# Kernel tuning notes

Measured on AMD Instinct MI355X. Metric: run time of the kernel, lower is better.

The kernel has to match this reference:

```python
import jax, jax.numpy as jnp
import numpy as np

N_NODES = 100_000
N_EDGES = 1_600_000
D = 128  # in = hidden = out channels
LAYERS = 3


def setup_inputs() -> dict:
    key = jax.random.key(0)
    ks = jax.random.split(key, 16)
    inp = {
        "x": jax.random.normal(ks[0], (N_NODES, D), dtype=jnp.float32),
        "edge_weight": jax.random.uniform(ks[1], (N_EDGES,), dtype=jnp.float32),
    }
    scale = 1.0 / np.sqrt(D)
    for l in range(LAYERS):
        inp[f"W_rel_{l}"] = jax.random.normal(ks[2 + 3 * l], (D, D), dtype=jnp.float32) * scale
        inp[f"W_root_{l}"] = jax.random.normal(ks[3 + 3 * l], (D, D), dtype=jnp.float32) * scale
        inp[f"b_{l}"] = jax.random.normal(ks[4 + 3 * l], (D,), dtype=jnp.float32) * scale
    inp["edge_src"] = jax.random.randint(ks[11], (N_EDGES,), 0, N_NODES, dtype=jnp.int32)
    inp["edge_dst"] = jax.random.randint(ks[12], (N_EDGES,), 0, N_NODES, dtype=jnp.int32)
    return inp


def _graph_conv(h, edge_src, edge_dst, edge_weight, W_rel, W_root, b):
    # PyG GraphConv: out_i = W_root @ h_i + W_rel @ (sum_{j->i} w_ji * h_j) + b
    msg = h[edge_src] * edge_weight[:, None]                      # [E, D] gather
    agg = jax.ops.segment_sum(msg, edge_dst, num_segments=h.shape[0])  # [N, D] scatter-add
    return agg @ W_rel.T + h @ W_root.T + b


def reference(x, edge_weight, W_rel_0, W_root_0, b_0, W_rel_1, W_root_1, b_1,
              W_rel_2, W_root_2, b_2, edge_src, edge_dst):
    h = _graph_conv(x, edge_src, edge_dst, edge_weight, W_rel_0, W_root_0, b_0)
    h = jax.nn.relu(h)
    h = _graph_conv(h, edge_src, edge_dst, edge_weight, W_rel_1, W_root_1, b_1)
    h = jax.nn.relu(h)
    h = _graph_conv(h, edge_src, edge_dst, edge_weight, W_rel_2, W_root_2, b_2)
    return h
```

## Files before the change

kernel.cpp:

```cpp
#include <hip/hip_runtime.h>

#define N_NODES 100000
#define N_EDGES 1600000
#define D 128
#define GEMM_GRID 6250
#define TILE_ROWS 16
#define BK_NODES 256
#define N_BUCKETS 391
#define BKT_CAP 5120
#define SC_BLOCKS 128
#define EPB 12500

typedef _Float16 f16;
typedef _Float16 f16x8 __attribute__((ext_vector_type(8)));
typedef _Float16 f16x2 __attribute__((ext_vector_type(2)));
typedef float f32x2 __attribute__((ext_vector_type(2)));
typedef float f32x4 __attribute__((ext_vector_type(4)));

__device__ __forceinline__ unsigned bf16bits(float x) {
    unsigned u = __float_as_uint(x);
    return ((u + 0x8000u) >> 16) & 0x7fffu;
}


__global__ __launch_bounds__(256) void bucket_scatter(const int* __restrict__ src,
                                                      const int* __restrict__ dst,
                                                      const float* __restrict__ w,
                                                      int* __restrict__ bcur,
                                                      int2* __restrict__ bkt) {
    __shared__ int hist[N_BUCKETS];
    __shared__ int base[N_BUCKETS];
    int tid = threadIdx.x;
    int v0  = blockIdx.x * (EPB / 4);
    const int4*   dst4 = (const int4*)dst;
    const int4*   src4 = (const int4*)src;
    const float4* w4   = (const float4*)w;

    for (int b = tid; b < N_BUCKETS; b += 256) hist[b] = 0;
    __syncthreads();

    for (int v = tid; v < EPB / 4; v += 256) {
        int4 d = dst4[v0 + v];
        atomicAdd(&hist[d.x >> 8], 1);
        atomicAdd(&hist[d.y >> 8], 1);
        atomicAdd(&hist[d.z >> 8], 1);
        atomicAdd(&hist[d.w >> 8], 1);
    }
    __syncthreads();

    for (int b = tid; b < N_BUCKETS; b += 256) {
        int c = hist[b];
        base[b] = b * BKT_CAP + ((c > 0) ? atomicAdd(&bcur[b], c) : 0);
        hist[b] = 0;
    }
    __syncthreads();

    for (int v = tid; v < EPB / 4; v += 256) {
        int4   d = dst4[v0 + v];
        int4   s = src4[v0 + v];
        float4 f = w4[v0 + v];
        {
            int p = base[d.x >> 8] + atomicAdd(&hist[d.x >> 8], 1);
            bkt[p] = make_int2(s.x, (int)(((unsigned)d.x << 15) | bf16bits(f.x)));
        }
        {
            int p = base[d.y >> 8] + atomicAdd(&hist[d.y >> 8], 1);
            bkt[p] = make_int2(s.y, (int)(((unsigned)d.y << 15) | bf16bits(f.y)));
        }
        {
            int p = base[d.z >> 8] + atomicAdd(&hist[d.z >> 8], 1);
            bkt[p] = make_int2(s.z, (int)(((unsigned)d.z << 15) | bf16bits(f.z)));
        }
        {
            int p = base[d.w >> 8] + atomicAdd(&hist[d.w >> 8], 1);
            bkt[p] = make_int2(s.w, (int)(((unsigned)d.w << 15) | bf16bits(f.w)));
        }
    }
}

__global__ __launch_bounds__(512) void bucket_scan(const int* __restrict__ bcnt,
                                                   int* __restrict__ bbase) {
    __shared__ int sc[512];
    int tid = threadIdx.x;
    int v = (tid < N_BUCKETS) ? bcnt[tid] : 0;
    sc[tid] = v;
    __syncthreads();
    for (int off = 1; off < 512; off <<= 1) {
        int t = (tid >= off) ? sc[tid - off] : 0;
        __syncthreads();
        sc[tid] += t;
        __syncthreads();
    }
    if (tid < N_BUCKETS) bbase[tid] = sc[tid] - v;
}

__global__ __launch_bounds__(256) void bucket_finalize(const int* __restrict__ bcnt,
                                                       const int* __restrict__ bbase,
                                                       const int2* __restrict__ bkt,
                                                       unsigned* __restrict__ csr,
                                                       int* __restrict__ row_ptr) {
    __shared__ int ncnt[BK_NODES];
    __shared__ int noff[BK_NODES];
    __shared__ int sc[BK_NODES];
    int tid   = threadIdx.x;
    int b     = blockIdx.x;
    int node0 = b * BK_NODES;
    int cnt   = bcnt[b];
    int base  = bbase[b];
    int e0    = b * BKT_CAP;

    ncnt[tid] = 0;
    __syncthreads();
    for (int i = tid; i < cnt; i += 256) {
        int local = (int)((unsigned)bkt[e0 + i].y >> 15) - node0;
        atomicAdd(&ncnt[local], 1);
    }
    __syncthreads();
    int s = ncnt[tid];
    sc[tid] = s;
    __syncthreads();
    for (int off = 1; off < 256; off <<= 1) {
        int t = (tid >= off) ? sc[tid - off] : 0;
        __syncthreads();
        sc[tid] += t;
        __syncthreads();
    }
    noff[tid] = sc[tid] - s;
    ncnt[tid] = 0;
    {
        int nN = N_NODES - node0; if (nN > BK_NODES) nN = BK_NODES;
        if (tid < nN) row_ptr[node0 + tid] = base + noff[tid];
        if (b == N_BUCKETS - 1 && tid == 0) row_ptr[N_NODES] = N_EDGES;
    }
    __syncthreads();
    for (int i = tid; i < cnt; i += 256) {
        int2 t = bkt[e0 + i];
        unsigned meta = (unsigned)t.y;
        int local = (int)(meta >> 15) - node0;
        int p = base + noff[local] + atomicAdd(&ncnt[local], 1);
        csr[p] = ((unsigned)t.x << 15) | (meta & 0x7fffu);
    }
}


__global__ __launch_bounds__(256) void cvt_x(const float* __restrict__ in,
                                             f16* __restrict__ out16,
                                             unsigned char* __restrict__ out8) {
    int i = blockIdx.x * 256 + threadIdx.x;
    const float4* in4 = (const float4*)in;
    float4 a = in4[i * 2], b = in4[i * 2 + 1];
    f16x8 v;
    v[0] = (f16)a.x; v[1] = (f16)a.y; v[2] = (f16)a.z; v[3] = (f16)a.w;
    v[4] = (f16)b.x; v[5] = (f16)b.y; v[6] = (f16)b.z; v[7] = (f16)b.w;
    ((f16x8*)out16)[i] = v;
    uint2 p8;
    int r = __builtin_amdgcn_cvt_pk_fp8_f32(a.x, a.y, 0, false);
    r     = __builtin_amdgcn_cvt_pk_fp8_f32(a.z, a.w, r, true);
    p8.x = (unsigned)r;
    r     = __builtin_amdgcn_cvt_pk_fp8_f32(b.x, b.y, 0, false);
    r     = __builtin_amdgcn_cvt_pk_fp8_f32(b.z, b.w, r, true);
    p8.y = (unsigned)r;
    ((uint2*)out8)[i] = p8;
}


__global__ __launch_bounds__(256) void pack_weights(const float* __restrict__ Wrel,
                                                    const float* __restrict__ Wroot,
                                                    f16* __restrict__ Bp) {
    int idx = blockIdx.x * 256 + threadIdx.x;
    int e = idx & 7, lane = (idx >> 3) & 63, ct = (idx >> 9) & 7, ks = idx >> 12;
    int j = ct * 16 + (lane & 15);
    int k = ks * 32 + (lane >> 4) * 8 + e;
    float w = (k < D) ? Wrel[j * D + k] : Wroot[j * D + (k - D)];
    Bp[idx] = (f16)w;
}


#define FMA8(CWV)                                                              \
    {                                                                          \
        float w = __uint_as_float(((CWV) & 0x7fffu) << 16);                    \
        f32x2 c0 = __builtin_amdgcn_cvt_pk_f32_fp8((int)rv[j].x, false);       \
        f32x2 c1 = __builtin_amdgcn_cvt_pk_f32_fp8((int)rv[j].x, true);        \
        f32x2 c2 = __builtin_amdgcn_cvt_pk_f32_fp8((int)rv[j].y, false);       \
        f32x2 c3 = __builtin_amdgcn_cvt_pk_f32_fp8((int)rv[j].y, true);        \
        a0 = fmaf(w, c0.x, a0); a1 = fmaf(w, c0.y, a1);                        \
        a2 = fmaf(w, c1.x, a2); a3 = fmaf(w, c1.y, a3);                        \
        a4 = fmaf(w, c2.x, a4); a5 = fmaf(w, c2.y, a5);                        \
        a6 = fmaf(w, c3.x, a6); a7 = fmaf(w, c3.y, a7);                        \
    }

template <int FINAL>
__global__ __launch_bounds__(256) void fused_layer(const f16* __restrict__ h,
                                                   const unsigned char* __restrict__ h8,
                                                   const int* __restrict__ row_ptr,
                                                   const unsigned* __restrict__ csr,
                                                   const f16x8* __restrict__ Bp,
                                                   const float* __restrict__ bias,
                                                   void* __restrict__ outp,
                                                   unsigned char* __restrict__ outp8) {
    __shared__ f16 sA[TILE_ROWS * 256];
    int tid  = threadIdx.x;
    int lane = tid & 63;
    int wid  = tid >> 6;
    int node0 = blockIdx.x * TILE_ROWS;
    const uint4* h16 = (const uint4*)h;

    int quad = lane >> 4;
    int ql   = lane & 15;
    unsigned qoff = (unsigned)ql * 8u;

    {
        int row  = wid * 4 + quad;
        int node = node0 + row;
        int beg = row_ptr[node], end = row_ptr[node + 1];

        float a0 = 0.f, a1 = 0.f, a2 = 0.f, a3 = 0.f;
        float a4 = 0.f, a5 = 0.f, a6 = 0.f, a7 = 0.f;

        int e = beg;
        unsigned cw[8];
        if (e + 8 <= end) {
#pragma unroll
            for (int j = 0; j < 8; ++j) cw[j] = csr[e + j];
        }
        while (e + 8 <= end) {
            uint2 rv[8];
            __builtin_amdgcn_sched_barrier(0);
#pragma unroll
            for (int j = 0; j < 8; ++j) {
                unsigned off = ((cw[j] >> 8) & 0xFFFFFF80u) | qoff;
                rv[j] = *(const uint2*)(h8 + off);
            }
            unsigned cwn[8];
            bool more = (e + 16 <= end);
            if (more) {
#pragma unroll
                for (int j = 0; j < 8; ++j) cwn[j] = csr[e + 8 + j];
            }
            __builtin_amdgcn_sched_barrier(0);
#pragma unroll
            for (int j = 0; j < 8; ++j) FMA8(cw[j]);
            if (more) {
#pragma unroll
                for (int j = 0; j < 8; ++j) cw[j] = cwn[j];
            }
            e += 8;
        }
        if (e < end) {
            int rem = end - e;
            int em1 = end - 1;
            unsigned sm[8];
            uint2 rv[8];
#pragma unroll
            for (int j = 0; j < 8; ++j) {
                int idx = e + j; idx = idx < em1 ? idx : em1;
                unsigned c = csr[idx];
                sm[j] = (j < rem) ? c : 0u;
            }
            __builtin_amdgcn_sched_barrier(0);
#pragma unroll
            for (int j = 0; j < 8; ++j) {
                unsigned off = ((sm[j] >> 8) & 0xFFFFFF80u) | qoff;
                rv[j] = *(const uint2*)(h8 + off);
            }
            __builtin_amdgcn_sched_barrier(0);
#pragma unroll
            for (int j = 0; j < 8; ++j) FMA8(sm[j]);
        }
        f16x8 ov;
        ov[0] = (f16)a0; ov[1] = (f16)a1; ov[2] = (f16)a2; ov[3] = (f16)a3;
        ov[4] = (f16)a4; ov[5] = (f16)a5; ov[6] = (f16)a6; ov[7] = (f16)a7;
        int o = (row * 256 + ql * 8) ^ ((row & 7) << 3);
        *(f16x8*)&sA[o] = ov;
    }

    {
        int r = tid >> 4, c8 = (tid & 15) + 16;
        int o = (r * 256 + c8 * 8) ^ ((r & 7) << 3);
        *(uint4*)&sA[o] = h16[(size_t)(node0 + r) * 16 + (c8 - 16)];
    }
    __syncthreads();

    float bv[2];
#pragma unroll
    for (int c = 0; c < 2; ++c) bv[c] = bias[wid * 32 + c * 16 + (lane & 15)];

    f32x4 acc[2] = {f32x4{0,0,0,0}, f32x4{0,0,0,0}};
    int arow = lane & 15;
    int kg   = (lane >> 4) * 8;

    f16x8 b0 = Bp[(0 * 8 + wid * 2 + 0) * 64 + lane];
    f16x8 b1 = Bp[(0 * 8 + wid * 2 + 1) * 64 + lane];
#pragma unroll 1
    for (int ks = 0; ks < 8; ++ks) {
        f16x8 n0, n1;
        if (ks < 7) {
            n0 = Bp[((ks + 1) * 8 + wid * 2 + 0) * 64 + lane];
            n1 = Bp[((ks + 1) * 8 + wid * 2 + 1) * 64 + lane];
        }
        int o = (arow * 256 + ks * 32 + kg) ^ ((arow & 7) << 3);
        f16x8 afrag = *(const f16x8*)&sA[o];
        acc[0] = __builtin_amdgcn_mfma_f32_16x16x32_f16(afrag, b0, acc[0], 0, 0, 0);
        acc[1] = __builtin_amdgcn_mfma_f32_16x16x32_f16(afrag, b1, acc[1], 0, 0, 0);
        b0 = n0; b1 = n1;
    }

#pragma unroll
    for (int c = 0; c < 2; ++c) {
        int col = wid * 32 + c * 16 + (lane & 15);
#pragma unroll
        for (int r = 0; r < 4; ++r) {
            int row = node0 + (lane >> 4) * 4 + r;
            float o = acc[c][r] + bv[c];
            if (FINAL) {
                ((float*)outp)[(size_t)row * D + col] = o;
            } else {
                o = fmaxf(o, 0.f);
                ((f16*)outp)[(size_t)row * D + col] = (f16)o;
                int pk = __builtin_amdgcn_cvt_pk_fp8_f32(o, o, 0, false);
                outp8[(size_t)row * D + col] = (unsigned char)(pk & 0xff);
            }
        }
    }
}


extern "C" void kernel_launch(void* const* d_in, const int* in_sizes, int n_in,
                              void* d_out, int out_size, void* d_ws, size_t ws_size,
                              hipStream_t stream) {
    const float* x  = (const float*)d_in[0];
    const float* ew = (const float*)d_in[1];
    const float* W_rel[3]  = {(const float*)d_in[2], (const float*)d_in[5], (const float*)d_in[8]};
    const float* W_root[3] = {(const float*)d_in[3], (const float*)d_in[6], (const float*)d_in[9]};
    const float* bias[3]   = {(const float*)d_in[4], (const float*)d_in[7], (const float*)d_in[10]};
    const int* esrc = (const int*)d_in[11];
    const int* edst = (const int*)d_in[12];

    char* ws = (char*)d_ws;
    f16*           bufA16  = (f16*)           (ws);
    unsigned char* bufA8   = (unsigned char*) (ws + 25600000);
    f16*           bufB16  = (f16*)           (ws + 38400000);
    unsigned char* bufB8   = (unsigned char*) (ws + 64000000);
    unsigned*      csr     = (unsigned*)      (ws + 76800000);
    int2*          bkt     = (int2*)          (ws + 83200000);
    int*           row_ptr = (int*)           (ws + 99215360);
    int*           bcur    = (int*)           (ws + 99615376);
    int*           bbase   = (int*)           (ws + 99616940);
    f16*           Bp      = (f16*)           (ws + 99618504);

    hipMemsetAsync(bcur, 0, N_BUCKETS * sizeof(int), stream);
    bucket_scatter<<<SC_BLOCKS, 256, 0, stream>>>(esrc, edst, ew, bcur, bkt);
    bucket_scan<<<1, 512, 0, stream>>>(bcur, bbase);
    bucket_finalize<<<N_BUCKETS, 256, 0, stream>>>(bcur, bbase, bkt, csr, row_ptr);

    cvt_x<<<6250, 256, 0, stream>>>(x, bufA16, bufA8);
    for (int l = 0; l < 3; ++l)
        pack_weights<<<128, 256, 0, stream>>>(W_rel[l], W_root[l], Bp + l * 32768);

    fused_layer<0><<<GEMM_GRID, 256, 0, stream>>>(bufA16, bufA8, row_ptr, csr,
                                                  (const f16x8*)(Bp + 0 * 32768),
                                                  bias[0], bufB16, bufB8);
    fused_layer<0><<<GEMM_GRID, 256, 0, stream>>>(bufB16, bufB8, row_ptr, csr,
                                                  (const f16x8*)(Bp + 1 * 32768),
                                                  bias[1], bufA16, bufA8);
    fused_layer<1><<<GEMM_GRID, 256, 0, stream>>>(bufA16, bufA8, row_ptr, csr,
                                                  (const f16x8*)(Bp + 2 * 32768),
                                                  bias[2], d_out, nullptr);
}
```

Measured before the change: 216.0 us.

## Sort nodes by in-degree to balance gather work within fused layer tiles

Adds a counting sort of nodes by in-degree (histogram, scan, placement kernels) that builds a permutation. The fused layer kernels then process tiles of nodes with similar degree, so the quarter-waves that each gather one node's neighbours finish at about the same time instead of waiting on the slowest row. The cost is three extra small kernels, an extra perm lookup per row, and scattered row reads and output writes in place of contiguous ones.

```diff
diff --git a/kernel.cpp b/kernel.cpp
--- a/kernel.cpp
+++ b/kernel.cpp
@@ -10,6 +10,9 @@
 #define BKT_CAP 5120
 #define SC_BLOCKS 128
 #define EPB 12500
+#define DS_BLOCKS 25
+#define NPB 4000
+#define NBINS 32
 
 typedef _Float16 f16;
 typedef _Float16 f16x8 __attribute__((ext_vector_type(8)));
@@ -139,6 +142,62 @@
         int local = (int)(meta >> 15) - node0;
         int p = base + noff[local] + atomicAdd(&ncnt[local], 1);
         csr[p] = ((unsigned)t.x << 15) | (meta & 0x7fffu);
+    }
+}
+
+
+__global__ __launch_bounds__(1024) void degree_hist(const int* __restrict__ row_ptr,
+                                                    int* __restrict__ ghist) {
+    __shared__ int hist[NBINS];
+    int tid = threadIdx.x;
+    if (tid < NBINS) hist[tid] = 0;
+    __syncthreads();
+    int n0 = blockIdx.x * NPB;
+    for (int i = tid; i < NPB; i += 1024) {
+        int node = n0 + i;
+        int deg = row_ptr[node + 1] - row_ptr[node];
+        int bin = deg < NBINS - 1 ? deg : NBINS - 1;
+        atomicAdd(&hist[bin], 1);
+    }
+    __syncthreads();
+    if (tid < NBINS && hist[tid] > 0) atomicAdd(&ghist[tid], hist[tid]);
+}
+
+__global__ void bin_scan(const int* __restrict__ ghist, int* __restrict__ gcur) {
+    if (threadIdx.x == 0 && blockIdx.x == 0) {
+        int run = 0;
+        for (int b = 0; b < NBINS; ++b) { gcur[b] = run; run += ghist[b]; }
+    }
+}
+
+__global__ __launch_bounds__(1024) void degree_place(const int* __restrict__ row_ptr,
+                                                     int* __restrict__ gcur,
+                                                     int* __restrict__ perm) {
+    __shared__ int hist[NBINS];
+    __shared__ int base[NBINS];
+    int tid = threadIdx.x;
+    if (tid < NBINS) hist[tid] = 0;
+    __syncthreads();
+    int n0 = blockIdx.x * NPB;
+    for (int i = tid; i < NPB; i += 1024) {
+        int node = n0 + i;
+        int deg = row_ptr[node + 1] - row_ptr[node];
+        int bin = deg < NBINS - 1 ? deg : NBINS - 1;
+        atomicAdd(&hist[bin], 1);
+    }
+    __syncthreads();
+    if (tid < NBINS) {
+        int c = hist[tid];
+        base[tid] = (c > 0) ? atomicAdd(&gcur[tid], c) : 0;
+        hist[tid] = 0;
+    }
+    __syncthreads();
+    for (int i = tid; i < NPB; i += 1024) {
+        int node = n0 + i;
+        int deg = row_ptr[node + 1] - row_ptr[node];
+        int bin = deg < NBINS - 1 ? deg : NBINS - 1;
+        int p = base[bin] + atomicAdd(&hist[bin], 1);
+        perm[p] = node;
     }
 }
 
@@ -194,6 +253,7 @@
                                                    const unsigned char* __restrict__ h8,
                                                    const int* __restrict__ row_ptr,
                                                    const unsigned* __restrict__ csr,
+                                                   const int* __restrict__ perm,
                                                    const f16x8* __restrict__ Bp,
                                                    const float* __restrict__ bias,
                                                    void* __restrict__ outp,
@@ -211,7 +271,7 @@
 
     {
         int row  = wid * 4 + quad;
-        int node = node0 + row;
+        int node = perm[node0 + row];
         int beg = row_ptr[node], end = row_ptr[node + 1];
 
         float a0 = 0.f, a1 = 0.f, a2 = 0.f, a3 = 0.f;
@@ -276,8 +336,9 @@
 
     {
         int r = tid >> 4, c8 = (tid & 15) + 16;
+        int nr = perm[node0 + r];
         int o = (r * 256 + c8 * 8) ^ ((r & 7) << 3);
-        *(uint4*)&sA[o] = h16[(size_t)(node0 + r) * 16 + (c8 - 16)];
+        *(uint4*)&sA[o] = h16[(size_t)nr * 16 + (c8 - 16)];
     }
     __syncthreads();
 
@@ -305,12 +366,15 @@
         b0 = n0; b1 = n1;
     }
 
+    int prow[4];
+#pragma unroll
+    for (int r = 0; r < 4; ++r) prow[r] = perm[node0 + (lane >> 4) * 4 + r];
 #pragma unroll
     for (int c = 0; c < 2; ++c) {
         int col = wid * 32 + c * 16 + (lane & 15);
 #pragma unroll
         for (int r = 0; r < 4; ++r) {
-            int row = node0 + (lane >> 4) * 4 + r;
+            int row = prow[r];
             float o = acc[c][r] + bv[c];
             if (FINAL) {
                 ((float*)outp)[(size_t)row * D + col] = o;
@@ -347,23 +411,31 @@
     int*           bcur    = (int*)           (ws + 99615376);
     int*           bbase   = (int*)           (ws + 99616940);
     f16*           Bp      = (f16*)           (ws + 99618504);
+    int*           perm    = (int*)           (ws + 99815112);
+    int*           ghist   = (int*)           (ws + 100215112);
+    int*           gcur    = (int*)           (ws + 100215240);
 
     hipMemsetAsync(bcur, 0, N_BUCKETS * sizeof(int), stream);
+    hipMemsetAsync(ghist, 0, NBINS * sizeof(int), stream);
     bucket_scatter<<<SC_BLOCKS, 256, 0, stream>>>(esrc, edst, ew, bcur, bkt);
     bucket_scan<<<1, 512, 0, stream>>>(bcur, bbase);
     bucket_finalize<<<N_BUCKETS, 256, 0, stream>>>(bcur, bbase, bkt, csr, row_ptr);
 
+    degree_hist<<<DS_BLOCKS, 1024, 0, stream>>>(row_ptr, ghist);
+    bin_scan<<<1, 32, 0, stream>>>(ghist, gcur);
+    degree_place<<<DS_BLOCKS, 1024, 0, stream>>>(row_ptr, gcur, perm);
+
     cvt_x<<<6250, 256, 0, stream>>>(x, bufA16, bufA8);
     for (int l = 0; l < 3; ++l)
         pack_weights<<<128, 256, 0, stream>>>(W_rel[l], W_root[l], Bp + l * 32768);
 
-    fused_layer<0><<<GEMM_GRID, 256, 0, stream>>>(bufA16, bufA8, row_ptr, csr,
+    fused_layer<0><<<GEMM_GRID, 256, 0, stream>>>(bufA16, bufA8, row_ptr, csr, perm,
                                                   (const f16x8*)(Bp + 0 * 32768),
                                                   bias[0], bufB16, bufB8);
-    fused_layer<0><<<GEMM_GRID, 256, 0, stream>>>(bufB16, bufB8, row_ptr, csr,
+    fused_layer<0><<<GEMM_GRID, 256, 0, stream>>>(bufB16, bufB8, row_ptr, csr, perm,
                                                   (const f16x8*)(Bp + 1 * 32768),
                                                   bias[1], bufA16, bufA8);
-    fused_layer<1><<<GEMM_GRID, 256, 0, stream>>>(bufA16, bufA8, row_ptr, csr,
+    fused_layer<1><<<GEMM_GRID, 256, 0, stream>>>(bufA16, bufA8, row_ptr, csr, perm,
                                                   (const f16x8*)(Bp + 2 * 32768),
                                                   bias[2], d_out, nullptr);
 }
```

Result: slower. 241.6 us (+11.9%).
